# Kernel optimization log

Measured on AMD Instinct MI355X. Metric: run time of the kernel, lower is better.

The kernel has to match this reference:

```python
import jax, jax.numpy as jnp
import numpy as np

NUM_HEADS = 16
ROT_DIM = 128  # == head_dim here
ROPE_BASE = 10000.0

def _deinterleave(t):
    # non-HF RoPE layout fix: cat(even channels, odd channels) along head_dim
    return jnp.concatenate([t[..., ::2], t[..., 1::2]], axis=-1)

def _rope(t, cos, sin):
    # t: [B,S,H,D]; rotary applied to first ROT_DIM dims with half-split (GPT-NeoX style)
    rot, rest = t[..., :ROT_DIM], t[..., ROT_DIM:]
    x1, x2 = rot[..., : ROT_DIM // 2], rot[..., ROT_DIM // 2 :]
    c = cos[None, :, None, :]
    s = sin[None, :, None, :]
    rot = jnp.concatenate([x1 * c - x2 * s, x1 * s + x2 * c], axis=-1)
    return jnp.concatenate([rot, rest], axis=-1) if rest.shape[-1] else rot

def setup_inputs() -> dict:
    key = jax.random.key(0)
    ks = jax.random.split(key, 5)
    B, S, E = 4, 2048, 2048
    return {
        "x": jax.random.normal(ks[0], (B, S, E), jnp.float32),
        "wqkv_w": jax.random.normal(ks[1], (3 * E, E), jnp.float32) * (E ** -0.5),
        "wqkv_b": jax.random.normal(ks[2], (3 * E,), jnp.float32) * 0.01,
        "wo_w": jax.random.normal(ks[3], (E, E), jnp.float32) * (E ** -0.5),
        "wo_b": jax.random.normal(ks[4], (E,), jnp.float32) * 0.01,
    }

def reference(x, wqkv_w, wqkv_b, wo_w, wo_b):
    B, S, E = x.shape
    H = NUM_HEADS
    D = E // H
    scale = 1.0 / jnp.sqrt(jnp.asarray(D, x.dtype))
    # fused QKV projection; channel layout is (h, three, d)
    qkv = x @ wqkv_w.T + wqkv_b               # [B,S,3E]
    qkv = qkv.reshape(B, S, H, 3, D)
    q, k, v = qkv[..., 0, :], qkv[..., 1, :], qkv[..., 2, :]  # [B,S,H,D]
    # non-HF rotary layout shuffle on q,k only
    q = _deinterleave(q)
    k = _deinterleave(k)
    # rotary embedding
    inv_freq = 1.0 / (ROPE_BASE ** (jnp.arange(0, ROT_DIM, 2, dtype=jnp.float32) / ROT_DIM))
    t = jnp.arange(S, dtype=jnp.float32)
    freqs = jnp.outer(t, inv_freq)            # [S, ROT_DIM/2]
    cos, sin = jnp.cos(freqs).astype(x.dtype), jnp.sin(freqs).astype(x.dtype)
    q = _rope(q, cos, sin)
    k = _rope(k, cos, sin)
    # causal self-attention (vanilla, fp32 softmax)
    scores = jnp.einsum("bshd,bthd->bhst", q, k) * scale   # [B,H,S,S]
    causal = jnp.tril(jnp.ones((S, S), bool))
    scores = jnp.where(causal[None, None], scores, jnp.asarray(-1e4, scores.dtype))
    attn = jax.nn.softmax(scores.astype(jnp.float32), axis=-1).astype(scores.dtype)
    ctx = jnp.einsum("bhst,bthd->bshd", attn, v)           # [B,S,H,D]
    # output projection
    out = ctx.reshape(B, S, E) @ wo_w.T + wo_b
    return out
```

## Files before the change

kernel.cpp:

```cpp
#include <hip/hip_runtime.h>


using frag_ab = __attribute__((ext_vector_type(8))) short;
using frag_cd = __attribute__((ext_vector_type(4))) float;

__device__ __forceinline__ float b2f(unsigned short u) {
  union { unsigned int i; float f; } v; v.i = ((unsigned int)u) << 16; return v.f;
}
__device__ __forceinline__ unsigned short f2b(float f) {
  union { float f; unsigned int i; } v; v.f = f;
  unsigned int r = v.i + 0x7FFFu + ((v.i >> 16) & 1u);
  return (unsigned short)(r >> 16);
}
__device__ __forceinline__ unsigned int pack2(float a, float b) {
  return (unsigned int)f2b(a) | ((unsigned int)f2b(b) << 16);
}
__device__ __forceinline__ void gload16(const unsigned short* g, unsigned short* l) {
  __builtin_amdgcn_global_load_lds(
      (const __attribute__((address_space(1))) unsigned int*)g,
      (__attribute__((address_space(3))) unsigned int*)l, 16, 0, 0);
}

__global__ __launch_bounds__(256)
void cvt_f32_bf16(const float* __restrict__ in, unsigned short* __restrict__ out) {
  long i = (long)(blockIdx.x * 256 + threadIdx.x) * 8;
  float4 a = *(const float4*)&in[i];
  float4 b = *(const float4*)&in[i + 4];
  uint4 p;
  p.x = pack2(a.x, a.y); p.y = pack2(a.z, a.w);
  p.z = pack2(b.x, b.y); p.w = pack2(b.z, b.w);
  *(uint4*)&out[i] = p;
}

__device__ __forceinline__ void stage_a_async(const unsigned short* A, unsigned short* As,
                                              int row0, int k0, int wave, int lane, int ldk) {
#pragma unroll
  for (int i = 0; i < 4; i++) {
    int rbase = wave * 32 + i * 8;
    int r = rbase + (lane >> 3);
    int srcc = (lane & 7) ^ (r & 7);
    gload16(&A[(long)(row0 + r) * ldk + k0 + srcc * 8], &As[rbase * 64]);
  }
}
__device__ __forceinline__ void stage_b_cvt(const float* Bw, unsigned short* Bs,
                                            int row0, int k0, int tid) {
#pragma unroll
  for (int i = 0; i < 4; i++) {
    int c = tid + i * 256;
    int r = c >> 3, ch = c & 7;
    const float* src = &Bw[(long)(row0 + r) * 2048 + k0 + ch * 8];
    float4 v0 = *(const float4*)src;
    float4 v1 = *(const float4*)(src + 4);
    uint4 p;
    p.x = pack2(v0.x, v0.y); p.y = pack2(v0.z, v0.w);
    p.z = pack2(v1.x, v1.y); p.w = pack2(v1.z, v1.w);
    *(uint4*)&Bs[r * 64 + ((ch ^ (r & 7)) * 8)] = p;
  }
}

__global__ __launch_bounds__(256)
void gemm_qkv(const unsigned short* __restrict__ A,
              const float* __restrict__ Bw,
              const unsigned short* __restrict__ Bbf,
              const float* __restrict__ bias,
              unsigned short* __restrict__ Qb,
              unsigned short* __restrict__ Kb,
              unsigned short* __restrict__ Vt) {
  __shared__ __align__(16) unsigned short As[128 * 64];
  __shared__ __align__(16) unsigned short Bs[128 * 64];
  const int tid  = threadIdx.x;
  const int wave = tid >> 6, lane = tid & 63;
  const int quad = lane >> 4, l16 = lane & 15;
  const int wm = (wave & 1) * 64, wn = (wave >> 1) * 64;
  const int row0A = blockIdx.x * 128;
  const int row0B = blockIdx.y * 128;

  frag_cd acc[4][4];
#pragma unroll
  for (int i = 0; i < 4; i++)
#pragma unroll
    for (int j = 0; j < 4; j++) acc[i][j] = (frag_cd){0.f, 0.f, 0.f, 0.f};

  for (int k0 = 0; k0 < 2048; k0 += 64) {
    stage_a_async(A, As, row0A, k0, wave, lane, 2048);
    if (Bbf) stage_a_async(Bbf, Bs, row0B, k0, wave, lane, 2048);
    else     stage_b_cvt(Bw, Bs, row0B, k0, tid);
    __syncthreads();
#pragma unroll
    for (int kk = 0; kk < 64; kk += 32) {
      frag_ab af[4], bf[4];
#pragma unroll
      for (int mi = 0; mi < 4; mi++) {
        int row = wm + mi * 16 + l16;
        af[mi] = *(const frag_ab*)&As[row * 64 + (((quad + (kk >> 3)) ^ (l16 & 7)) * 8)];
      }
#pragma unroll
      for (int ni = 0; ni < 4; ni++) {
        int row = wn + ni * 16 + l16;
        bf[ni] = *(const frag_ab*)&Bs[row * 64 + (((quad + (kk >> 3)) ^ (l16 & 7)) * 8)];
      }
#pragma unroll
      for (int mi = 0; mi < 4; mi++)
#pragma unroll
        for (int ni = 0; ni < 4; ni++)
          acc[mi][ni] = __builtin_amdgcn_mfma_f32_16x16x32_bf16(af[mi], bf[ni], acc[mi][ni], 0, 0, 0);
    }
    __syncthreads();
  }
#pragma unroll
  for (int ni = 0; ni < 4; ni++) {
    int col  = row0B + wn + ni * 16 + l16;
    int h    = col / 384;
    int rem  = col - h * 384;
    int slot = rem >> 7;
    int d    = rem & 127;
    float bv = bias[col];
#pragma unroll
    for (int mi = 0; mi < 4; mi++) {
#pragma unroll
      for (int r = 0; r < 4; r++) {
        int row = row0A + wm + mi * 16 + quad * 4 + r;
        int b = row >> 11, s = row & 2047;
        unsigned short val = f2b(acc[mi][ni][r] + bv);
        if (slot == 0)      Qb[((long)(b * 16 + h) * 2048 + s) * 128 + d] = val;
        else if (slot == 1) Kb[((long)(b * 16 + h) * 2048 + s) * 128 + d] = val;
        else                Vt[((long)(b * 16 + h) * 128 + d) * 2048 + s] = val;
      }
    }
  }
}

__global__ __launch_bounds__(256)
void rope_inplace(unsigned short* __restrict__ Qb, unsigned short* __restrict__ Kb) {
  int wid  = blockIdx.x * 4 + (threadIdx.x >> 6);
  int j    = threadIdx.x & 63;
  int part = wid & 1;
  int s    = (wid >> 1) & 2047;
  int bh   = wid >> 12;
  unsigned short* buf = part ? Kb : Qb;
  long base = ((long)bh * 2048 + s) * 128;
  unsigned int pr = *(const unsigned int*)&buf[base + 2 * j];
  float x1 = b2f((unsigned short)(pr & 0xFFFFu));
  float x2 = b2f((unsigned short)(pr >> 16));
  float inv = powf(10000.0f, -(float)(2 * j) / 128.0f);
  float ang = (float)s * inv;
  float sn, cs;
  sincosf(ang, &sn, &cs);
  float sc = part ? 1.0f : 0.08838834764831845f;
  cs *= sc; sn *= sc;
  buf[base + j]      = f2b(x1 * cs - x2 * sn);
  buf[base + 64 + j] = f2b(x1 * sn + x2 * cs);
}

__global__ __launch_bounds__(256)
void attn_fwd(const unsigned short* __restrict__ Q,
              const unsigned short* __restrict__ K,
              const unsigned short* __restrict__ Vt,
              unsigned short* __restrict__ ctx) {
  __shared__ __align__(16) unsigned short Ks[64 * 128];
  __shared__ __align__(16) unsigned short Vs[128 * 64];
  __shared__ __align__(16) unsigned short Ps[4][32 * 72];
  const int bh = blockIdx.x;
  const int tid = threadIdx.x;
  const int wave = tid >> 6, lane = tid & 63;
  const int quad = lane >> 4, l16 = lane & 15;
  const long base  = (long)bh * 2048 * 128;
  const long vbase = (long)bh * 262144;
  const int b = bh >> 4, h = bh & 15;
  unsigned short* pw = &Ps[wave][0];

  for (int pass = 0; pass < 2; ++pass) {
    const int qt = pass ? (15 - blockIdx.y) : blockIdx.y;
    const int q0 = qt * 128 + wave * 32;

    frag_ab qf[2][4];
#pragma unroll
    for (int mi = 0; mi < 2; mi++)
#pragma unroll
      for (int ks = 0; ks < 4; ks++)
        qf[mi][ks] = *(const frag_ab*)&Q[base + (long)(q0 + mi * 16 + l16) * 128 + ks * 32 + quad * 8];

    frag_cd o[2][8];
#pragma unroll
    for (int mi = 0; mi < 2; mi++)
#pragma unroll
      for (int ni = 0; ni < 8; ni++) o[mi][ni] = (frag_cd){0.f, 0.f, 0.f, 0.f};
    float m_i[2][4], l_i[2][4];
#pragma unroll
    for (int mi = 0; mi < 2; mi++)
#pragma unroll
      for (int r = 0; r < 4; r++) { m_i[mi][r] = -1.0e30f; l_i[mi][r] = 0.f; }

    const int kv_end = qt * 128 + 128;
    for (int kv0 = 0; kv0 < kv_end; kv0 += 64) {
      __syncthreads();
#pragma unroll
      for (int i = 0; i < 4; i++) {
        int rbase = (wave * 4 + i) * 4;
        int r = rbase + (lane >> 4);
        int srcc = (lane & 15) ^ (r & 15);
        gload16(&K[base + (long)(kv0 + r) * 128 + srcc * 8], &Ks[rbase * 128]);
      }
#pragma unroll
      for (int i = 0; i < 4; i++) {
        int rbase = wave * 32 + i * 8;
        int r = rbase + (lane >> 3);
        int srcc = (lane & 7) ^ (r & 7);
        gload16(&Vt[vbase + (long)r * 2048 + kv0 + srcc * 8], &Vs[rbase * 64]);
      }
      __syncthreads();

      if (kv0 <= q0 + 31) {
        float p[2][4][4];
        __builtin_amdgcn_s_setprio(1);
#pragma unroll
        for (int nj = 0; nj < 4; nj++) {
          frag_ab kf[4];
          int row = nj * 16 + l16;
#pragma unroll
          for (int ks = 0; ks < 4; ks++)
            kf[ks] = *(const frag_ab*)&Ks[row * 128 + (((ks * 4 + quad) ^ (row & 15)) * 8)];
#pragma unroll
          for (int mi = 0; mi < 2; mi++) {
            frag_cd acc = (frag_cd){0.f, 0.f, 0.f, 0.f};
#pragma unroll
            for (int ks = 0; ks < 4; ks++)
              acc = __builtin_amdgcn_mfma_f32_16x16x32_bf16(qf[mi][ks], kf[ks], acc, 0, 0, 0);
            int colg = kv0 + nj * 16 + l16;
#pragma unroll
            for (int r = 0; r < 4; r++) {
              int rowg = q0 + mi * 16 + quad * 4 + r;
              p[mi][nj][r] = (colg <= rowg) ? acc[r] : -10000.0f;
            }
          }
        }
        __builtin_amdgcn_s_setprio(0);

#pragma unroll
        for (int mi = 0; mi < 2; mi++) {
#pragma unroll
          for (int r = 0; r < 4; r++) {
            float mx = fmaxf(fmaxf(p[mi][0][r], p[mi][1][r]), fmaxf(p[mi][2][r], p[mi][3][r]));
#pragma unroll
            for (int off = 1; off < 16; off <<= 1)
              mx = fmaxf(mx, __shfl_xor(mx, off, 64));
            float mnew  = fmaxf(m_i[mi][r], mx);
            float alpha = __expf(m_i[mi][r] - mnew);
            float rs = 0.f;
#pragma unroll
            for (int nj = 0; nj < 4; nj++) {
              float e = __expf(p[mi][nj][r] - mnew);
              p[mi][nj][r] = e;
              rs += e;
            }
#pragma unroll
            for (int off = 1; off < 16; off <<= 1)
              rs += __shfl_xor(rs, off, 64);
            l_i[mi][r] = l_i[mi][r] * alpha + rs;
            m_i[mi][r] = mnew;
#pragma unroll
            for (int ni = 0; ni < 8; ni++) o[mi][ni][r] *= alpha;
          }
        }

#pragma unroll
        for (int mi = 0; mi < 2; mi++)
#pragma unroll
          for (int nj = 0; nj < 4; nj++)
#pragma unroll
            for (int r = 0; r < 4; r++)
              pw[(mi * 16 + quad * 4 + r) * 72 + nj * 16 + l16] = f2b(p[mi][nj][r]);

        __builtin_amdgcn_s_setprio(1);
#pragma unroll
        for (int ni = 0; ni < 8; ni++) {
          int vrow = ni * 16 + l16;
          frag_ab vf0 = *(const frag_ab*)&Vs[vrow * 64 + ((quad ^ (l16 & 7)) * 8)];
          frag_ab vf1 = *(const frag_ab*)&Vs[vrow * 64 + (((quad + 4) ^ (l16 & 7)) * 8)];
#pragma unroll
          for (int mi = 0; mi < 2; mi++) {
            frag_ab pf0 = *(const frag_ab*)&pw[(mi * 16 + l16) * 72 + quad * 8];
            frag_ab pf1 = *(const frag_ab*)&pw[(mi * 16 + l16) * 72 + 32 + quad * 8];
            o[mi][ni] = __builtin_amdgcn_mfma_f32_16x16x32_bf16(pf0, vf0, o[mi][ni], 0, 0, 0);
            o[mi][ni] = __builtin_amdgcn_mfma_f32_16x16x32_bf16(pf1, vf1, o[mi][ni], 0, 0, 0);
          }
        }
        __builtin_amdgcn_s_setprio(0);
      }
    }

#pragma unroll
    for (int mi = 0; mi < 2; mi++) {
#pragma unroll
      for (int r = 0; r < 4; r++) {
        float inv = 1.0f / fmaxf(l_i[mi][r], 1.0e-20f);
        int s = q0 + mi * 16 + quad * 4 + r;
        long rowb = ((long)b * 2048 + s) * 2048 + h * 128;
#pragma unroll
        for (int ni = 0; ni < 8; ni++)
          ctx[rowb + ni * 16 + l16] = f2b(o[mi][ni][r] * inv);
      }
    }
  }
}

__global__ __launch_bounds__(256)
void gemm_ctx(const unsigned short* __restrict__ A,
              const float* __restrict__ Bw,
              const unsigned short* __restrict__ Bbf,
              const float* __restrict__ bias,
              float* __restrict__ C) {
  __shared__ __align__(16) unsigned short As[128 * 64];
  __shared__ __align__(16) unsigned short Bs[128 * 64];
  const int tid  = threadIdx.x;
  const int wave = tid >> 6, lane = tid & 63;
  const int quad = lane >> 4, l16 = lane & 15;
  const int wm = (wave & 1) * 64, wn = (wave >> 1) * 64;
  const int row0A = blockIdx.x * 128;
  const int row0B = blockIdx.y * 128;

  frag_cd acc[4][4];
#pragma unroll
  for (int i = 0; i < 4; i++)
#pragma unroll
    for (int j = 0; j < 4; j++) acc[i][j] = (frag_cd){0.f, 0.f, 0.f, 0.f};

  for (int k0 = 0; k0 < 2048; k0 += 64) {
    stage_a_async(A, As, row0A, k0, wave, lane, 2048);
    if (Bbf) stage_a_async(Bbf, Bs, row0B, k0, wave, lane, 2048);
    else     stage_b_cvt(Bw, Bs, row0B, k0, tid);
    __syncthreads();
#pragma unroll
    for (int kk = 0; kk < 64; kk += 32) {
      frag_ab af[4], bf[4];
#pragma unroll
      for (int mi = 0; mi < 4; mi++) {
        int row = wm + mi * 16 + l16;
        af[mi] = *(const frag_ab*)&As[row * 64 + (((quad + (kk >> 3)) ^ (l16 & 7)) * 8)];
      }
#pragma unroll
      for (int ni = 0; ni < 4; ni++) {
        int row = wn + ni * 16 + l16;
        bf[ni] = *(const frag_ab*)&Bs[row * 64 + (((quad + (kk >> 3)) ^ (l16 & 7)) * 8)];
      }
#pragma unroll
      for (int mi = 0; mi < 4; mi++)
#pragma unroll
        for (int ni = 0; ni < 4; ni++)
          acc[mi][ni] = __builtin_amdgcn_mfma_f32_16x16x32_bf16(af[mi], bf[ni], acc[mi][ni], 0, 0, 0);
    }
    __syncthreads();
  }
#pragma unroll
  for (int ni = 0; ni < 4; ni++) {
    int col = row0B + wn + ni * 16 + l16;
    float bv = bias[col];
#pragma unroll
    for (int mi = 0; mi < 4; mi++) {
#pragma unroll
      for (int r = 0; r < 4; r++) {
        int row = row0A + wm + mi * 16 + quad * 4 + r;
        C[(long)row * 2048 + col] = acc[mi][ni][r] + bv;
      }
    }
  }
}

extern "C" void kernel_launch(void* const* d_in, const int* in_sizes, int n_in,
                              void* d_out, int out_size, void* d_ws, size_t ws_size,
                              hipStream_t stream) {
  const float* x      = (const float*)d_in[0];
  const float* wqkv_w = (const float*)d_in[1];
  const float* wqkv_b = (const float*)d_in[2];
  const float* wo_w   = (const float*)d_in[3];
  const float* wo_b   = (const float*)d_in[4];

  unsigned short* xb  = (unsigned short*)d_out;
  unsigned short* Qb  = (unsigned short*)d_out + 16777216;
  unsigned short* Kb  = (unsigned short*)d_ws;
  unsigned short* Vt  = (unsigned short*)d_ws + 16777216;
  unsigned short* ctx = (unsigned short*)d_out;
  float* outf = (float*)d_ws;

  const bool big = ws_size >= 100663296UL;
  unsigned short* Wq = big ? (unsigned short*)d_ws + 33554432 : nullptr;
  unsigned short* Wo = big ? (unsigned short*)d_ws + 46137344 : nullptr;

  cvt_f32_bf16<<<8192, 256, 0, stream>>>(x, xb);
  if (big) {
    cvt_f32_bf16<<<6144, 256, 0, stream>>>(wqkv_w, Wq);
    cvt_f32_bf16<<<2048, 256, 0, stream>>>(wo_w, Wo);
  }
  gemm_qkv<<<dim3(64, 48), 256, 0, stream>>>(xb, wqkv_w, Wq, wqkv_b, Qb, Kb, Vt);
  rope_inplace<<<65536, 256, 0, stream>>>(Qb, Kb);
  attn_fwd<<<dim3(64, 8), 256, 0, stream>>>(Qb, Kb, Vt, ctx);
  gemm_ctx<<<dim3(64, 16), 256, 0, stream>>>(ctx, wo_w, Wo, wo_b, outf);
  hipMemcpyAsync(d_out, outf, 67108864UL, hipMemcpyDeviceToDevice, stream);
}
```

Measured before the change: 798.8 us.

## Add triple-buffered 256x128 async-LDS GEMMs for QKV and output projections

```diff
diff --git a/kernel.cpp b/kernel.cpp
--- a/kernel.cpp
+++ b/kernel.cpp
@@ -30,6 +30,14 @@
   p.x = pack2(a.x, a.y); p.y = pack2(a.z, a.w);
   p.z = pack2(b.x, b.y); p.w = pack2(b.z, b.w);
   *(uint4*)&out[i] = p;
+}
+
+__device__ __forceinline__ void stage_round512(const unsigned short* G, unsigned short* Ls,
+                                               int row0, int k0, int rr0,
+                                               int wave, int lane) {
+  int r = rr0 + wave * 8 + (lane >> 3);
+  int srcc = (lane & 7) ^ (r & 7);
+  gload16(&G[(long)(row0 + r) * 2048 + k0 + srcc * 8], &Ls[(rr0 + wave * 8) * 64]);
 }
 
 __device__ __forceinline__ void stage_a_async(const unsigned short* A, unsigned short* As,
@@ -55,6 +63,288 @@
     p.x = pack2(v0.x, v0.y); p.y = pack2(v0.z, v0.w);
     p.z = pack2(v1.x, v1.y); p.w = pack2(v1.z, v1.w);
     *(uint4*)&Bs[r * 64 + ((ch ^ (r & 7)) * 8)] = p;
+  }
+}
+
+__global__ __launch_bounds__(512, 2)
+void gemm_qkv2(const unsigned short* __restrict__ A,
+               const unsigned short* __restrict__ Bbf,
+               const float* __restrict__ bias,
+               unsigned short* __restrict__ Qb,
+               unsigned short* __restrict__ Kb,
+               unsigned short* __restrict__ Vt) {
+  __shared__ __align__(16) unsigned short As[3][256 * 64];
+  __shared__ __align__(16) unsigned short Bs[3][128 * 64];
+  const int tid  = threadIdx.x;
+  const int wave = tid >> 6, lane = tid & 63;
+  const int quad = lane >> 4, l16 = lane & 15;
+  const int wr = wave >> 1, wc = wave & 1;
+  const int row0A = blockIdx.x * 256;
+  const int row0B = blockIdx.y * 128;
+
+  frag_cd acc[4][4];
+#pragma unroll
+  for (int i = 0; i < 4; i++)
+#pragma unroll
+    for (int j = 0; j < 4; j++) acc[i][j] = (frag_cd){0.f, 0.f, 0.f, 0.f};
+
+#pragma unroll
+  for (int tt = 0; tt < 2; ++tt) {
+    stage_round512(A,   As[tt], row0A, tt * 64, 0,   wave, lane);
+    stage_round512(A,   As[tt], row0A, tt * 64, 64,  wave, lane);
+    stage_round512(A,   As[tt], row0A, tt * 64, 128, wave, lane);
+    stage_round512(A,   As[tt], row0A, tt * 64, 192, wave, lane);
+    stage_round512(Bbf, Bs[tt], row0B, tt * 64, 0,   wave, lane);
+    stage_round512(Bbf, Bs[tt], row0B, tt * 64, 64,  wave, lane);
+  }
+  asm volatile("s_waitcnt vmcnt(6)" ::: "memory");
+  __builtin_amdgcn_s_barrier();
+
+  int cur = 0;
+  for (int t = 0; t < 32; ++t) {
+    const unsigned short* as = As[cur];
+    const unsigned short* bs = Bs[cur];
+    int nxt2 = cur + 2; if (nxt2 >= 3) nxt2 -= 3;
+    const int k2 = (t + 2) * 64;
+    const bool pf = (t < 30);
+
+#define LDA_(mi, k2i) (*(const frag_ab*)&as[(wr * 64 + (mi) * 16 + l16) * 64 + ((((k2i) * 4 + quad) ^ (l16 & 7)) * 8)])
+#define LDB_(ni, k2i) (*(const frag_ab*)&bs[(wc * 64 + (ni) * 16 + l16) * 64 + ((((k2i) * 4 + quad) ^ (l16 & 7)) * 8)])
+
+    frag_ab a0[2][2], a1[2][2], b0[2][2], b1[2][2];
+
+    if (pf) {
+      stage_round512(A, As[nxt2], row0A, k2, 0,  wave, lane);
+      stage_round512(A, As[nxt2], row0A, k2, 64, wave, lane);
+    }
+#pragma unroll
+    for (int k2i = 0; k2i < 2; k2i++)
+#pragma unroll
+      for (int i = 0; i < 2; i++) { a0[k2i][i] = LDA_(i, k2i); b0[k2i][i] = LDB_(i, k2i); }
+    __builtin_amdgcn_s_barrier();
+    __builtin_amdgcn_s_setprio(1);
+#pragma unroll
+    for (int k2i = 0; k2i < 2; k2i++)
+#pragma unroll
+      for (int i = 0; i < 2; i++)
+#pragma unroll
+        for (int j = 0; j < 2; j++)
+          acc[i][j] = __builtin_amdgcn_mfma_f32_16x16x32_bf16(a0[k2i][i], b0[k2i][j], acc[i][j], 0, 0, 0);
+    __builtin_amdgcn_s_setprio(0);
+    __builtin_amdgcn_s_barrier();
+
+    if (pf) {
+      stage_round512(A, As[nxt2], row0A, k2, 128, wave, lane);
+      stage_round512(A, As[nxt2], row0A, k2, 192, wave, lane);
+    }
+#pragma unroll
+    for (int k2i = 0; k2i < 2; k2i++)
+#pragma unroll
+      for (int j = 0; j < 2; j++) b1[k2i][j] = LDB_(2 + j, k2i);
+    __builtin_amdgcn_s_barrier();
+    __builtin_amdgcn_s_setprio(1);
+#pragma unroll
+    for (int k2i = 0; k2i < 2; k2i++)
+#pragma unroll
+      for (int i = 0; i < 2; i++)
+#pragma unroll
+        for (int j = 0; j < 2; j++)
+          acc[i][2 + j] = __builtin_amdgcn_mfma_f32_16x16x32_bf16(a0[k2i][i], b1[k2i][j], acc[i][2 + j], 0, 0, 0);
+    __builtin_amdgcn_s_setprio(0);
+    __builtin_amdgcn_s_barrier();
+
+    if (pf) stage_round512(Bbf, Bs[nxt2], row0B, k2, 0, wave, lane);
+#pragma unroll
+    for (int k2i = 0; k2i < 2; k2i++)
+#pragma unroll
+      for (int i = 0; i < 2; i++) a1[k2i][i] = LDA_(2 + i, k2i);
+    __builtin_amdgcn_s_barrier();
+    __builtin_amdgcn_s_setprio(1);
+#pragma unroll
+    for (int k2i = 0; k2i < 2; k2i++)
+#pragma unroll
+      for (int i = 0; i < 2; i++)
+#pragma unroll
+        for (int j = 0; j < 2; j++)
+          acc[2 + i][j] = __builtin_amdgcn_mfma_f32_16x16x32_bf16(a1[k2i][i], b0[k2i][j], acc[2 + i][j], 0, 0, 0);
+    __builtin_amdgcn_s_setprio(0);
+    __builtin_amdgcn_s_barrier();
+
+    if (pf) stage_round512(Bbf, Bs[nxt2], row0B, k2, 64, wave, lane);
+    __builtin_amdgcn_s_barrier();
+    __builtin_amdgcn_s_setprio(1);
+#pragma unroll
+    for (int k2i = 0; k2i < 2; k2i++)
+#pragma unroll
+      for (int i = 0; i < 2; i++)
+#pragma unroll
+        for (int j = 0; j < 2; j++)
+          acc[2 + i][2 + j] = __builtin_amdgcn_mfma_f32_16x16x32_bf16(a1[k2i][i], b1[k2i][j], acc[2 + i][2 + j], 0, 0, 0);
+    __builtin_amdgcn_s_setprio(0);
+    if (t < 30) asm volatile("s_waitcnt vmcnt(6)" ::: "memory");
+    else        asm volatile("s_waitcnt vmcnt(0)" ::: "memory");
+    __builtin_amdgcn_s_barrier();
+#undef LDA_
+#undef LDB_
+    cur = cur + 1; if (cur == 3) cur = 0;
+  }
+
+#pragma unroll
+  for (int ni = 0; ni < 4; ni++) {
+    int col  = row0B + wc * 64 + ni * 16 + l16;
+    int h    = col / 384;
+    int rem  = col - h * 384;
+    int slot = rem >> 7;
+    int d    = rem & 127;
+    float bv = bias[col];
+#pragma unroll
+    for (int mi = 0; mi < 4; mi++) {
+#pragma unroll
+      for (int r = 0; r < 4; r++) {
+        int row = row0A + wr * 64 + mi * 16 + quad * 4 + r;
+        int b = row >> 11, s = row & 2047;
+        unsigned short val = f2b(acc[mi][ni][r] + bv);
+        if (slot == 0)      Qb[((long)(b * 16 + h) * 2048 + s) * 128 + d] = val;
+        else if (slot == 1) Kb[((long)(b * 16 + h) * 2048 + s) * 128 + d] = val;
+        else                Vt[((long)(b * 16 + h) * 128 + d) * 2048 + s] = val;
+      }
+    }
+  }
+}
+
+__global__ __launch_bounds__(512, 2)
+void gemm_ctx2(const unsigned short* __restrict__ A,
+               const unsigned short* __restrict__ Bbf,
+               const float* __restrict__ bias,
+               float* __restrict__ C) {
+  __shared__ __align__(16) unsigned short As[3][256 * 64];
+  __shared__ __align__(16) unsigned short Bs[3][128 * 64];
+  const int tid  = threadIdx.x;
+  const int wave = tid >> 6, lane = tid & 63;
+  const int quad = lane >> 4, l16 = lane & 15;
+  const int wr = wave >> 1, wc = wave & 1;
+  const int row0A = blockIdx.x * 256;
+  const int row0B = blockIdx.y * 128;
+
+  frag_cd acc[4][4];
+#pragma unroll
+  for (int i = 0; i < 4; i++)
+#pragma unroll
+    for (int j = 0; j < 4; j++) acc[i][j] = (frag_cd){0.f, 0.f, 0.f, 0.f};
+
+#pragma unroll
+  for (int tt = 0; tt < 2; ++tt) {
+    stage_round512(A,   As[tt], row0A, tt * 64, 0,   wave, lane);
+    stage_round512(A,   As[tt], row0A, tt * 64, 64,  wave, lane);
+    stage_round512(A,   As[tt], row0A, tt * 64, 128, wave, lane);
+    stage_round512(A,   As[tt], row0A, tt * 64, 192, wave, lane);
+    stage_round512(Bbf, Bs[tt], row0B, tt * 64, 0,   wave, lane);
+    stage_round512(Bbf, Bs[tt], row0B, tt * 64, 64,  wave, lane);
+  }
+  asm volatile("s_waitcnt vmcnt(6)" ::: "memory");
+  __builtin_amdgcn_s_barrier();
+
+  int cur = 0;
+  for (int t = 0; t < 32; ++t) {
+    const unsigned short* as = As[cur];
+    const unsigned short* bs = Bs[cur];
+    int nxt2 = cur + 2; if (nxt2 >= 3) nxt2 -= 3;
+    const int k2 = (t + 2) * 64;
+    const bool pf = (t < 30);
+
+#define LDA_(mi, k2i) (*(const frag_ab*)&as[(wr * 64 + (mi) * 16 + l16) * 64 + ((((k2i) * 4 + quad) ^ (l16 & 7)) * 8)])
+#define LDB_(ni, k2i) (*(const frag_ab*)&bs[(wc * 64 + (ni) * 16 + l16) * 64 + ((((k2i) * 4 + quad) ^ (l16 & 7)) * 8)])
+
+    frag_ab a0[2][2], a1[2][2], b0[2][2], b1[2][2];
+
+    if (pf) {
+      stage_round512(A, As[nxt2], row0A, k2, 0,  wave, lane);
+      stage_round512(A, As[nxt2], row0A, k2, 64, wave, lane);
+    }
+#pragma unroll
+    for (int k2i = 0; k2i < 2; k2i++)
+#pragma unroll
+      for (int i = 0; i < 2; i++) { a0[k2i][i] = LDA_(i, k2i); b0[k2i][i] = LDB_(i, k2i); }
+    __builtin_amdgcn_s_barrier();
+    __builtin_amdgcn_s_setprio(1);
+#pragma unroll
+    for (int k2i = 0; k2i < 2; k2i++)
+#pragma unroll
+      for (int i = 0; i < 2; i++)
+#pragma unroll
+        for (int j = 0; j < 2; j++)
+          acc[i][j] = __builtin_amdgcn_mfma_f32_16x16x32_bf16(a0[k2i][i], b0[k2i][j], acc[i][j], 0, 0, 0);
+    __builtin_amdgcn_s_setprio(0);
+    __builtin_amdgcn_s_barrier();
+
+    if (pf) {
+      stage_round512(A, As[nxt2], row0A, k2, 128, wave, lane);
+      stage_round512(A, As[nxt2], row0A, k2, 192, wave, lane);
+    }
+#pragma unroll
+    for (int k2i = 0; k2i < 2; k2i++)
+#pragma unroll
+      for (int j = 0; j < 2; j++) b1[k2i][j] = LDB_(2 + j, k2i);
+    __builtin_amdgcn_s_barrier();
+    __builtin_amdgcn_s_setprio(1);
+#pragma unroll
+    for (int k2i = 0; k2i < 2; k2i++)
+#pragma unroll
+      for (int i = 0; i < 2; i++)
+#pragma unroll
+        for (int j = 0; j < 2; j++)
+          acc[i][2 + j] = __builtin_amdgcn_mfma_f32_16x16x32_bf16(a0[k2i][i], b1[k2i][j], acc[i][2 + j], 0, 0, 0);
+    __builtin_amdgcn_s_setprio(0);
+    __builtin_amdgcn_s_barrier();
+
+    if (pf) stage_round512(Bbf, Bs[nxt2], row0B, k2, 0, wave, lane);
+#pragma unroll
+    for (int k2i = 0; k2i < 2; k2i++)
+#pragma unroll
+      for (int i = 0; i < 2; i++) a1[k2i][i] = LDA_(2 + i, k2i);
+    __builtin_amdgcn_s_barrier();
+    __builtin_amdgcn_s_setprio(1);
+#pragma unroll
+    for (int k2i = 0; k2i < 2; k2i++)
+#pragma unroll
+      for (int i = 0; i < 2; i++)
+#pragma unroll
+        for (int j = 0; j < 2; j++)
+          acc[2 + i][j] = __builtin_amdgcn_mfma_f32_16x16x32_bf16(a1[k2i][i], b0[k2i][j], acc[2 + i][j], 0, 0, 0);
+    __builtin_amdgcn_s_setprio(0);
+    __builtin_amdgcn_s_barrier();
+
+    if (pf) stage_round512(Bbf, Bs[nxt2], row0B, k2, 64, wave, lane);
+    __builtin_amdgcn_s_barrier();
+    __builtin_amdgcn_s_setprio(1);
+#pragma unroll
+    for (int k2i = 0; k2i < 2; k2i++)
+#pragma unroll
+      for (int i = 0; i < 2; i++)
+#pragma unroll
+        for (int j = 0; j < 2; j++)
+          acc[2 + i][2 + j] = __builtin_amdgcn_mfma_f32_16x16x32_bf16(a1[k2i][i], b1[k2i][j], acc[2 + i][2 + j], 0, 0, 0);
+    __builtin_amdgcn_s_setprio(0);
+    if (t < 30) asm volatile("s_waitcnt vmcnt(6)" ::: "memory");
+    else        asm volatile("s_waitcnt vmcnt(0)" ::: "memory");
+    __builtin_amdgcn_s_barrier();
+#undef LDA_
+#undef LDB_
+    cur = cur + 1; if (cur == 3) cur = 0;
+  }
+
+#pragma unroll
+  for (int ni = 0; ni < 4; ni++) {
+    int col = row0B + wc * 64 + ni * 16 + l16;
+    float bv = bias[col];
+#pragma unroll
+    for (int mi = 0; mi < 4; mi++) {
+#pragma unroll
+      for (int r = 0; r < 4; r++) {
+        int row = row0A + wr * 64 + mi * 16 + quad * 4 + r;
+        C[(long)row * 2048 + col] = acc[mi][ni][r] + bv;
+      }
+    }
   }
 }
 
@@ -391,9 +681,11 @@
     cvt_f32_bf16<<<6144, 256, 0, stream>>>(wqkv_w, Wq);
     cvt_f32_bf16<<<2048, 256, 0, stream>>>(wo_w, Wo);
   }
-  gemm_qkv<<<dim3(64, 48), 256, 0, stream>>>(xb, wqkv_w, Wq, wqkv_b, Qb, Kb, Vt);
+  if (big) gemm_qkv2<<<dim3(32, 48), 512, 0, stream>>>(xb, Wq, wqkv_b, Qb, Kb, Vt);
+  else     gemm_qkv<<<dim3(64, 48), 256, 0, stream>>>(xb, wqkv_w, nullptr, wqkv_b, Qb, Kb, Vt);
   rope_inplace<<<65536, 256, 0, stream>>>(Qb, Kb);
   attn_fwd<<<dim3(64, 8), 256, 0, stream>>>(Qb, Kb, Vt, ctx);
-  gemm_ctx<<<dim3(64, 16), 256, 0, stream>>>(ctx, wo_w, Wo, wo_b, outf);
+  if (big) gemm_ctx2<<<dim3(32, 16), 512, 0, stream>>>(ctx, Wo, wo_b, outf);
+  else     gemm_ctx<<<dim3(64, 16), 256, 0, stream>>>(ctx, wo_w, nullptr, wo_b, outf);
   hipMemcpyAsync(d_out, outf, 67108864UL, hipMemcpyDeviceToDevice, stream);
 }
```

Result: slower. 1.013 ms (+26.8%).

## Compute transposed S tile so softmax reduces in-lane with fewer shuffles

Applied to the files above, without the earlier changes.

```diff
diff --git a/kernel.cpp b/kernel.cpp
--- a/kernel.cpp
+++ b/kernel.cpp
@@ -3,6 +3,7 @@
 
 using frag_ab = __attribute__((ext_vector_type(8))) short;
 using frag_cd = __attribute__((ext_vector_type(4))) float;
+typedef __attribute__((ext_vector_type(2))) unsigned int uint2v;
 
 __device__ __forceinline__ float b2f(unsigned short u) {
   union { unsigned int i; float f; } v; v.i = ((unsigned int)u) << 16; return v.f;
@@ -159,7 +160,7 @@
               unsigned short* __restrict__ ctx) {
   __shared__ __align__(16) unsigned short Ks[64 * 128];
   __shared__ __align__(16) unsigned short Vs[128 * 64];
-  __shared__ __align__(16) unsigned short Ps[4][32 * 72];
+  __shared__ __align__(16) unsigned short Ps[4][32 * 64];
   const int bh = blockIdx.x;
   const int tid = threadIdx.x;
   const int wave = tid >> 6, lane = tid & 63;
@@ -185,11 +186,8 @@
     for (int mi = 0; mi < 2; mi++)
 #pragma unroll
       for (int ni = 0; ni < 8; ni++) o[mi][ni] = (frag_cd){0.f, 0.f, 0.f, 0.f};
-    float m_i[2][4], l_i[2][4];
-#pragma unroll
-    for (int mi = 0; mi < 2; mi++)
-#pragma unroll
-      for (int r = 0; r < 4; r++) { m_i[mi][r] = -1.0e30f; l_i[mi][r] = 0.f; }
+    float m_i[2] = {-1.0e30f, -1.0e30f};
+    float l_i[2] = {0.f, 0.f};
 
     const int kv_end = qt * 128 + 128;
     for (int kv0 = 0; kv0 < kv_end; kv0 += 64) {
@@ -214,9 +212,9 @@
         float p[2][4][4];
         __builtin_amdgcn_s_setprio(1);
 #pragma unroll
-        for (int nj = 0; nj < 4; nj++) {
+        for (int kt = 0; kt < 4; kt++) {
           frag_ab kf[4];
-          int row = nj * 16 + l16;
+          int row = kt * 16 + l16;
 #pragma unroll
           for (int ks = 0; ks < 4; ks++)
             kf[ks] = *(const frag_ab*)&Ks[row * 128 + (((ks * 4 + quad) ^ (row & 15)) * 8)];
@@ -225,52 +223,87 @@
             frag_cd acc = (frag_cd){0.f, 0.f, 0.f, 0.f};
 #pragma unroll
             for (int ks = 0; ks < 4; ks++)
-              acc = __builtin_amdgcn_mfma_f32_16x16x32_bf16(qf[mi][ks], kf[ks], acc, 0, 0, 0);
-            int colg = kv0 + nj * 16 + l16;
+              acc = __builtin_amdgcn_mfma_f32_16x16x32_bf16(kf[ks], qf[mi][ks], acc, 0, 0, 0);
+#pragma unroll
+            for (int r = 0; r < 4; r++) p[mi][kt][r] = acc[r];
+          }
+        }
+        __builtin_amdgcn_s_setprio(0);
+
+        if (kv0 + 63 > q0) {
+#pragma unroll
+          for (int mi = 0; mi < 2; mi++) {
+            int qg = q0 + mi * 16 + l16;
+#pragma unroll
+            for (int kt = 0; kt < 4; kt++)
+#pragma unroll
+              for (int r = 0; r < 4; r++) {
+                int kvg = kv0 + kt * 16 + quad * 4 + r;
+                if (kvg > qg) p[mi][kt][r] = -10000.0f;
+              }
+          }
+        }
+
+        float alpha[2];
+#pragma unroll
+        for (int mi = 0; mi < 2; mi++) {
+          float mx = -1.0e30f;
+#pragma unroll
+          for (int kt = 0; kt < 4; kt++)
+            mx = fmaxf(mx, fmaxf(fmaxf(p[mi][kt][0], p[mi][kt][1]),
+                                 fmaxf(p[mi][kt][2], p[mi][kt][3])));
+          mx = fmaxf(mx, __shfl_xor(mx, 16, 64));
+          mx = fmaxf(mx, __shfl_xor(mx, 32, 64));
+          float mnew = fmaxf(m_i[mi], mx);
+          alpha[mi] = __expf(m_i[mi] - mnew);
+          m_i[mi] = mnew;
+          float rs = 0.f;
+#pragma unroll
+          for (int kt = 0; kt < 4; kt++)
 #pragma unroll
             for (int r = 0; r < 4; r++) {
-              int rowg = q0 + mi * 16 + quad * 4 + r;
-              p[mi][nj][r] = (colg <= rowg) ? acc[r] : -10000.0f;
-            }
-          }
-        }
-        __builtin_amdgcn_s_setprio(0);
-
-#pragma unroll
-        for (int mi = 0; mi < 2; mi++) {
-#pragma unroll
-          for (int r = 0; r < 4; r++) {
-            float mx = fmaxf(fmaxf(p[mi][0][r], p[mi][1][r]), fmaxf(p[mi][2][r], p[mi][3][r]));
-#pragma unroll
-            for (int off = 1; off < 16; off <<= 1)
-              mx = fmaxf(mx, __shfl_xor(mx, off, 64));
-            float mnew  = fmaxf(m_i[mi][r], mx);
-            float alpha = __expf(m_i[mi][r] - mnew);
-            float rs = 0.f;
-#pragma unroll
-            for (int nj = 0; nj < 4; nj++) {
-              float e = __expf(p[mi][nj][r] - mnew);
-              p[mi][nj][r] = e;
+              float e = __expf(p[mi][kt][r] - mnew);
+              p[mi][kt][r] = e;
               rs += e;
             }
-#pragma unroll
-            for (int off = 1; off < 16; off <<= 1)
-              rs += __shfl_xor(rs, off, 64);
-            l_i[mi][r] = l_i[mi][r] * alpha + rs;
-            m_i[mi][r] = mnew;
-#pragma unroll
-            for (int ni = 0; ni < 8; ni++) o[mi][ni][r] *= alpha;
+          rs += __shfl_xor(rs, 16, 64);
+          rs += __shfl_xor(rs, 32, 64);
+          l_i[mi] = l_i[mi] * alpha[mi] + rs;
+        }
+
+        if (!(__all(alpha[0] == 1.0f) && __all(alpha[1] == 1.0f))) {
+#pragma unroll
+          for (int mi = 0; mi < 2; mi++) {
+            float ar[4];
+#pragma unroll
+            for (int r = 0; r < 4; r++) ar[r] = __shfl(alpha[mi], quad * 4 + r, 64);
+#pragma unroll
+            for (int ni = 0; ni < 8; ni++)
+#pragma unroll
+              for (int r = 0; r < 4; r++) o[mi][ni][r] *= ar[r];
           }
         }
 
 #pragma unroll
+        for (int mi = 0; mi < 2; mi++) {
+          int row = mi * 16 + l16;
+#pragma unroll
+          for (int kt = 0; kt < 4; kt++) {
+            unsigned int u0 = pack2(p[mi][kt][0], p[mi][kt][1]);
+            unsigned int u1 = pack2(p[mi][kt][2], p[mi][kt][3]);
+            int ch = kt * 2 + (quad >> 1);
+            int addr = row * 64 + ((ch ^ (l16 & 7)) * 8) + (quad & 1) * 4;
+            *(uint2v*)&pw[addr] = (uint2v){u0, u1};
+          }
+        }
+
+        frag_ab pf[2][2];
+#pragma unroll
         for (int mi = 0; mi < 2; mi++)
 #pragma unroll
-          for (int nj = 0; nj < 4; nj++)
-#pragma unroll
-            for (int r = 0; r < 4; r++)
-              pw[(mi * 16 + quad * 4 + r) * 72 + nj * 16 + l16] = f2b(p[mi][nj][r]);
-
+          for (int ks = 0; ks < 2; ks++)
+            pf[mi][ks] = *(const frag_ab*)&pw[(mi * 16 + l16) * 64 +
+                                              (((ks * 4 + quad) ^ (l16 & 7)) * 8)];
         __builtin_amdgcn_s_setprio(1);
 #pragma unroll
         for (int ni = 0; ni < 8; ni++) {
@@ -279,10 +312,8 @@
           frag_ab vf1 = *(const frag_ab*)&Vs[vrow * 64 + (((quad + 4) ^ (l16 & 7)) * 8)];
 #pragma unroll
           for (int mi = 0; mi < 2; mi++) {
-            frag_ab pf0 = *(const frag_ab*)&pw[(mi * 16 + l16) * 72 + quad * 8];
-            frag_ab pf1 = *(const frag_ab*)&pw[(mi * 16 + l16) * 72 + 32 + quad * 8];
-            o[mi][ni] = __builtin_amdgcn_mfma_f32_16x16x32_bf16(pf0, vf0, o[mi][ni], 0, 0, 0);
-            o[mi][ni] = __builtin_amdgcn_mfma_f32_16x16x32_bf16(pf1, vf1, o[mi][ni], 0, 0, 0);
+            o[mi][ni] = __builtin_amdgcn_mfma_f32_16x16x32_bf16(pf[mi][0], vf0, o[mi][ni], 0, 0, 0);
+            o[mi][ni] = __builtin_amdgcn_mfma_f32_16x16x32_bf16(pf[mi][1], vf1, o[mi][ni], 0, 0, 0);
           }
         }
         __builtin_amdgcn_s_setprio(0);
@@ -291,9 +322,10 @@
 
 #pragma unroll
     for (int mi = 0; mi < 2; mi++) {
+      float rl = 1.0f / fmaxf(l_i[mi], 1.0e-20f);
 #pragma unroll
       for (int r = 0; r < 4; r++) {
-        float inv = 1.0f / fmaxf(l_i[mi][r], 1.0e-20f);
+        float inv = __shfl(rl, quad * 4 + r, 64);
         int s = q0 + mi * 16 + quad * 4 + r;
         long rowb = ((long)b * 2048 + s) * 2048 + h * 128;
 #pragma unroll
```

Measured after the change: 735.7 us. 7.9% less time.
